# Performance work log

Hardware: AMD Instinct MI355X
Metric: run time of the kernel (lower is better)

## Reference

```python
import jax, jax.numpy as jnp
import numpy as np

ALPHA = 2.0
BETA = 50.0
BASE = 0.5
MARGIN = 0.1

B, D = 8192, 128
NUM_CLASSES = 512


def setup_inputs() -> dict:
    key = jax.random.key(0)
    k1, k2 = jax.random.split(key)
    emb = jax.random.normal(k1, (B, D), dtype=jnp.float32)
    emb = emb / jnp.linalg.norm(emb, axis=1, keepdims=True)  # unit-norm embeddings (standard for MS loss)
    labels = jax.random.randint(k2, (B,), 0, NUM_CLASSES, dtype=jnp.int64)
    return {"emb": emb, "labels": labels}


def reference(emb, labels):
    # sim: [B, B] similarity matrix
    sim = emb @ emb.T
    n = emb.shape[0]
    eq = labels[:, None] == labels[None, :]
    eye = jnp.eye(n, dtype=bool)
    pos = eq & ~eye          # positive pairs, diagonal removed
    neg = ~eq                # negative pairs

    # per-row hard-mining thresholds
    pos_min = jnp.min(jnp.where(pos, sim, jnp.inf), axis=1)    # min positive sim per row
    neg_max = jnp.max(jnp.where(neg, sim, -jnp.inf), axis=1)   # max negative sim per row

    neg_hard = neg & (sim + MARGIN > pos_min[:, None])
    pos_hard = pos & (sim - MARGIN < neg_max[:, None])

    # fallback: if mining selects nothing in a row, use all pos/neg (matches torch code)
    neg_sel = jnp.where(jnp.any(neg_hard, axis=1, keepdims=True), neg_hard, neg)
    pos_sel = jnp.where(jnp.any(pos_hard, axis=1, keepdims=True), pos_hard, pos)

    pos_loss = jnp.log1p(jnp.sum(jnp.where(pos_sel, jnp.exp(-ALPHA * (sim - BASE)), 0.0), axis=1)) / ALPHA
    neg_loss = jnp.log1p(jnp.sum(jnp.where(neg_sel, jnp.exp(BETA * (sim - BASE)), 0.0), axis=1)) / BETA

    valid = jnp.any(pos, axis=1) & jnp.any(neg, axis=1)  # rows skipped in torch loop
    row_loss = pos_loss + neg_loss
    num_valid = jnp.maximum(jnp.sum(valid.astype(jnp.float32)), 1.0)
    return jnp.sum(jnp.where(valid, row_loss, 0.0)) / num_valid
```

## Files before the change

kernel.cpp:

```cpp
#include <hip/hip_runtime.h>
#include <hip/hip_bf16.h>

#define NROW 8192
#define NDIM 128
#define CTILE 64
#define CCHUNK 8
#define RBLK 128
#define CAP 64
#define NCLS 512

typedef __attribute__((ext_vector_type(8))) short short8;
typedef __attribute__((ext_vector_type(4))) float f32x4;
typedef __attribute__((address_space(1))) const unsigned int guint;
typedef __attribute__((address_space(3))) unsigned int luint;

__device__ __forceinline__ unsigned f2u_mono(float f) {
  unsigned u = __float_as_uint(f);
  return (u & 0x80000000u) ? ~u : (u | 0x80000000u);
}
__device__ __forceinline__ float u2f_mono(unsigned u) {
  return __uint_as_float((u & 0x80000000u) ? (u ^ 0x80000000u) : ~u);
}
__device__ __forceinline__ unsigned short f2bf(float f) {
  unsigned u = __float_as_uint(f);
  u += 0x7fffu + ((u >> 16) & 1u);
  return (unsigned short)(u >> 16);
}

__global__ __launch_bounds__(256) void k_pre(
    const float* __restrict__ emb, const int* __restrict__ labels,
    unsigned short* __restrict__ h,
    unsigned* __restrict__ nmaxu, float* __restrict__ anb, float* __restrict__ hnb,
    float* __restrict__ pmin, float* __restrict__ apb, int* __restrict__ rcnt,
    float* __restrict__ pcache, unsigned* __restrict__ done_partial) {
  __shared__ float Le[CAP][NDIM + 1];
  __shared__ int rows_s[CAP];
  __shared__ int scnt;

  const int t = threadIdx.x;
  const int c = blockIdx.x;
  const int gid = c * 256 + t;

  if (gid < NROW) {
    nmaxu[gid] = 0u;
    anb[gid] = 0.f;
    hnb[gid] = 0.f;
  }
  if (c == 0 && t < 3) done_partial[t] = 0u;

  {
    int i = gid * 8;
    float4 f0 = *reinterpret_cast<const float4*>(emb + i);
    float4 f1 = *reinterpret_cast<const float4*>(emb + i + 4);
    ushort4 a, b;
    a.x = f2bf(f0.x); a.y = f2bf(f0.y); a.z = f2bf(f0.z); a.w = f2bf(f0.w);
    b.x = f2bf(f1.x); b.y = f2bf(f1.y); b.z = f2bf(f1.z); b.w = f2bf(f1.w);
    *reinterpret_cast<ushort4*>(h + i) = a;
    *reinterpret_cast<ushort4*>(h + i + 4) = b;
  }

  if (t == 0) scnt = 0;
  __syncthreads();
#pragma unroll
  for (int it = 0; it < NROW / 256; ++it) {
    const int row = it * 256 + t;
    if (labels[row] == c) {
      const int idx = atomicAdd(&scnt, 1);
      if (idx < CAP) rows_s[idx] = row;
    }
  }
  __syncthreads();
  const int cnt = min(scnt, CAP);
  if (cnt == 0) return;

  for (int idx = t; idx < cnt * NDIM; idx += 256) {
    const int k = idx >> 7, d = idx & 127;
    Le[k][d] = emb[(size_t)rows_s[k] * NDIM + d];
  }
  __syncthreads();

  const int il = t >> 4, jl = t & 15;
  for (int ib = 0; ib < cnt; ib += 16) {
    const int i = ib + il;
    float pm = INFINITY, apv = 0.f;
    for (int jb = 0; jb < cnt; jb += 16) {
      const int j = jb + jl;
      float p = INFINITY;
      if (i < cnt && j < cnt) {
        if (i != j) {
          float s = 0.f;
#pragma unroll 8
          for (int d = 0; d < NDIM; ++d) s = fmaf(Le[i][d], Le[j][d], s);
          p = s;
        }
        pcache[(size_t)rows_s[i] * CAP + j] = p;
        if (i != j) {
          pm = fminf(pm, p);
          apv += exp2f(fmaf(p, -2.885390082f, 1.442695041f));
        }
      }
    }
    pm = fminf(pm, __shfl_xor(pm, 1)); pm = fminf(pm, __shfl_xor(pm, 2));
    pm = fminf(pm, __shfl_xor(pm, 4)); pm = fminf(pm, __shfl_xor(pm, 8));
    apv += __shfl_xor(apv, 1); apv += __shfl_xor(apv, 2);
    apv += __shfl_xor(apv, 4); apv += __shfl_xor(apv, 8);
    if (jl == 0 && i < cnt) {
      pmin[rows_s[i]] = pm;
      apb[rows_s[i]] = apv;
      rcnt[rows_s[i]] = cnt;
    }
  }
}

__device__ __forceinline__ void stage_tile(const unsigned short* __restrict__ eh,
                                           int colBase, int t,
                                           unsigned short* __restrict__ Lbuf) {
#pragma unroll
  for (int it = 0; it < 4; ++it) {
    const int idx = it * 256 + t;
    const int r = idx >> 4;
    const int c = idx & 15;
    const int q = c ^ (r & 15);
    const unsigned short* src = eh + (size_t)(colBase + r) * NDIM + q * 8;
    unsigned short* dst = Lbuf + r * NDIM + c * 8;
    __builtin_amdgcn_global_load_lds((guint*)src, (luint*)dst, 16, 0, 0);
  }
}

__device__ __forceinline__ void mfma_from_lds(const unsigned short* __restrict__ Lbuf,
                                              const short8 (&bv)[4][2],
                                              const f32x4& Z,
                                              int g, int l15,
                                              f32x4 (&acc)[4][2]) {
#pragma unroll
  for (int kk = 0; kk < 4; ++kk) {
    short8 av[4];
#pragma unroll
    for (int m = 0; m < 4; ++m) {
      const int R = m * 16 + l15;
      const int pc = (kk * 4 + g) ^ l15;
      av[m] = *reinterpret_cast<const short8*>(Lbuf + R * NDIM + pc * 8);
    }
#pragma unroll
    for (int m = 0; m < 4; ++m)
#pragma unroll
      for (int n = 0; n < 2; ++n)
        acc[m][n] = __builtin_amdgcn_mfma_f32_16x16x32_bf16(
            av[m], bv[kk][n], (kk == 0) ? Z : acc[m][n], 0, 0, 0);
  }
}

__global__ __launch_bounds__(256, 3) void k_neg(
    const unsigned short* __restrict__ eh, const int* __restrict__ labels,
    const float* __restrict__ pmin, unsigned* __restrict__ nmaxu,
    float* __restrict__ anb, float* __restrict__ hnb) {
  __shared__ unsigned short L[2][CTILE * NDIM];

  const int t = threadIdx.x;
  const int lane = t & 63;
  const int wid = t >> 6;
  const int g = lane >> 4;
  const int l15 = lane & 15;
  const int rowBase = blockIdx.y * RBLK;
  const int col0 = blockIdx.x * CCHUNK * CTILE;

  stage_tile(eh, col0, t, L[0]);

  short8 bv[4][2];
  int lr[2];
  float thrn[2];
#pragma unroll
  for (int n = 0; n < 2; ++n) {
    const int grow = rowBase + wid * 32 + n * 16 + l15;
    lr[n] = labels[grow];
    thrn[n] = pmin[grow] - 0.1f;
#pragma unroll
    for (int kk = 0; kk < 4; ++kk)
      bv[kk][n] = *reinterpret_cast<const short8*>(eh + (size_t)grow * NDIM + kk * 32 + g * 8);
  }

  float nmaxA[2] = {-INFINITY, -INFINITY};
  float anA[2] = {0.f, 0.f}, hnA[2] = {0.f, 0.f};
  const f32x4 Z = {0.f, 0.f, 0.f, 0.f};

  asm volatile("s_waitcnt vmcnt(0)");
  __syncthreads();

  f32x4 acc[4][2];
  int cur = 0;
  for (int tt = 0; tt < CCHUNK; ++tt) {
    const int colBase = col0 + tt * CTILE;
    if (tt + 1 < CCHUNK) stage_tile(eh, colBase + CTILE, t, L[cur ^ 1]);
    int4 lcv[4];
#pragma unroll
    for (int m = 0; m < 4; ++m)
      lcv[m] = *reinterpret_cast<const int4*>(labels + colBase + m * 16 + g * 4);
    mfma_from_lds(L[cur], bv, Z, g, l15, acc);
#pragma unroll
    for (int n = 0; n < 2; ++n) {
#pragma unroll
      for (int m = 0; m < 4; ++m) {
#pragma unroll
        for (int r = 0; r < 4; ++r) {
          const float s = acc[m][n][r];
          const int lc = (r == 0) ? lcv[m].x : (r == 1) ? lcv[m].y
                        : (r == 2) ? lcv[m].z : lcv[m].w;
          const float x = (lr[n] == lc) ? -INFINITY : s;
          nmaxA[n] = fmaxf(nmaxA[n], x);
          const float e = exp2f(fmaf(x, 72.13475205f, -36.06737602f));
          anA[n] += e;
          hnA[n] += (x > thrn[n]) ? e : 0.f;
        }
      }
    }
    asm volatile("s_waitcnt vmcnt(0)");
    __syncthreads();
    cur ^= 1;
  }

#pragma unroll
  for (int n = 0; n < 2; ++n) {
    const int grow = rowBase + wid * 32 + n * 16 + l15;
    float nm = nmaxA[n], a0 = anA[n], a1 = hnA[n];
    nm = fmaxf(nm, __shfl_xor(nm, 16)); nm = fmaxf(nm, __shfl_xor(nm, 32));
    a0 += __shfl_xor(a0, 16); a0 += __shfl_xor(a0, 32);
    a1 += __shfl_xor(a1, 16); a1 += __shfl_xor(a1, 32);
    if (g == 0 && nm > -INFINITY) atomicMax(&nmaxu[grow], f2u_mono(nm));
    if (g == 1 && a0 > 0.f) atomicAdd(&anb[grow], a0);
    if (g == 2 && a1 > 0.f) atomicAdd(&hnb[grow], a1);
  }
}

__global__ __launch_bounds__(256) void k_final(
    const int* __restrict__ rcnt, const unsigned* __restrict__ nmaxu,
    const float* __restrict__ pcache, const float* __restrict__ apb,
    const float* __restrict__ anb, const float* __restrict__ hnb,
    unsigned* __restrict__ done_partial, float* __restrict__ out) {
  unsigned* done = done_partial;
  float* partial = (float*)(done_partial + 1);
  const int t = threadIdx.x;
  const int row = blockIdx.x * 256 + t;
  const int cnt = min(rcnt[row], CAP);
  const float thrp = u2f_mono(nmaxu[row]) + 0.1f;
  float hp = 0.f;
  for (int j = 0; j < cnt; ++j) {
    const float p = pcache[(size_t)row * CAP + j];
    hp += (p < thrp) ? exp2f(fmaf(p, -2.885390082f, 1.442695041f)) : 0.f;
  }
  const float ap = apb[row], an = anb[row], hn = hnb[row];
  const bool valid = (ap > 0.f) && (an > 0.f);
  const float ps = (hp > 0.f) ? hp : ap;
  const float ns = (hn > 0.f) ? hn : an;
  float acc = valid ? (0.5f * log1pf(ps) + 0.02f * log1pf(ns)) : 0.f;
  float cntv = valid ? 1.f : 0.f;
#pragma unroll
  for (int o = 32; o > 0; o >>= 1) {
    acc += __shfl_down(acc, o);
    cntv += __shfl_down(cntv, o);
  }
  __shared__ float sa[4], sc[4];
  const int w = t >> 6, lane = t & 63;
  if (lane == 0) { sa[w] = acc; sc[w] = cntv; }
  __syncthreads();
  if (t == 0) {
    atomicAdd(&partial[0], sa[0] + sa[1] + sa[2] + sa[3]);
    atomicAdd(&partial[1], sc[0] + sc[1] + sc[2] + sc[3]);
    __threadfence();
    if (atomicAdd(done, 1u) == (unsigned)(NROW / 256 - 1)) {
      const float A = atomicAdd(&partial[0], 0.f);
      const float C = atomicAdd(&partial[1], 0.f);
      out[0] = A / fmaxf(C, 1.f);
    }
  }
}

extern "C" void kernel_launch(void* const* d_in, const int* in_sizes, int n_in,
                              void* d_out, int out_size, void* d_ws, size_t ws_size,
                              hipStream_t stream) {
  const float* emb = (const float*)d_in[0];
  const int* labels = (const int*)d_in[1];
  float* out = (float*)d_out;

  unsigned short* embh = (unsigned short*)d_ws;
  float* pmin = (float*)((char*)d_ws + (size_t)NROW * NDIM * 2);
  float* apb = pmin + NROW;
  unsigned* nmaxu = (unsigned*)(apb + NROW);
  float* anb = (float*)(nmaxu + NROW);
  float* hnb = anb + NROW;
  int* rcnt = (int*)(hnb + NROW);
  unsigned* done_partial = (unsigned*)(rcnt + NROW);
  float* pcache = (float*)(done_partial + 4);

  k_pre<<<NCLS, 256, 0, stream>>>(emb, labels, embh, nmaxu, anb, hnb,
                                  pmin, apb, rcnt, pcache, done_partial);
  dim3 grid(NROW / (CTILE * CCHUNK), NROW / RBLK);
  k_neg<<<grid, 256, 0, stream>>>(embh, labels, pmin, nmaxu, anb, hnb);
  k_final<<<NROW / 256, 256, 0, stream>>>(rcnt, nmaxu, pcache,
                                          apb, anb, hnb, done_partial, out);
}
```

Measured before the change: 66.68 us.

## Restructure k_neg into single-wave blocks with barrier-free vmcnt-gated double buffering

```diff
diff --git a/kernel.cpp b/kernel.cpp
--- a/kernel.cpp
+++ b/kernel.cpp
@@ -3,9 +3,9 @@
 
 #define NROW 8192
 #define NDIM 128
-#define CTILE 64
-#define CCHUNK 8
-#define RBLK 128
+#define CTILE 32
+#define NTILE 16
+#define RWAVE 64
 #define CAP 64
 #define NCLS 512
 
@@ -116,8 +116,8 @@
                                            int colBase, int t,
                                            unsigned short* __restrict__ Lbuf) {
 #pragma unroll
-  for (int it = 0; it < 4; ++it) {
-    const int idx = it * 256 + t;
+  for (int it = 0; it < 8; ++it) {
+    const int idx = it * 64 + t;
     const int r = idx >> 4;
     const int c = idx & 15;
     const int q = c ^ (r & 15);
@@ -127,79 +127,79 @@
   }
 }
 
-__device__ __forceinline__ void mfma_from_lds(const unsigned short* __restrict__ Lbuf,
-                                              const short8 (&bv)[4][2],
-                                              const f32x4& Z,
-                                              int g, int l15,
-                                              f32x4 (&acc)[4][2]) {
-#pragma unroll
-  for (int kk = 0; kk < 4; ++kk) {
-    short8 av[4];
-#pragma unroll
-    for (int m = 0; m < 4; ++m) {
-      const int R = m * 16 + l15;
-      const int pc = (kk * 4 + g) ^ l15;
-      av[m] = *reinterpret_cast<const short8*>(Lbuf + R * NDIM + pc * 8);
-    }
-#pragma unroll
-    for (int m = 0; m < 4; ++m)
-#pragma unroll
-      for (int n = 0; n < 2; ++n)
-        acc[m][n] = __builtin_amdgcn_mfma_f32_16x16x32_bf16(
-            av[m], bv[kk][n], (kk == 0) ? Z : acc[m][n], 0, 0, 0);
-  }
-}
-
-__global__ __launch_bounds__(256, 3) void k_neg(
+__global__ __launch_bounds__(64) void k_neg(
     const unsigned short* __restrict__ eh, const int* __restrict__ labels,
     const float* __restrict__ pmin, unsigned* __restrict__ nmaxu,
     float* __restrict__ anb, float* __restrict__ hnb) {
   __shared__ unsigned short L[2][CTILE * NDIM];
 
   const int t = threadIdx.x;
-  const int lane = t & 63;
-  const int wid = t >> 6;
-  const int g = lane >> 4;
-  const int l15 = lane & 15;
-  const int rowBase = blockIdx.y * RBLK;
-  const int col0 = blockIdx.x * CCHUNK * CTILE;
-
-  stage_tile(eh, col0, t, L[0]);
-
-  short8 bv[4][2];
-  int lr[2];
-  float thrn[2];
-#pragma unroll
-  for (int n = 0; n < 2; ++n) {
-    const int grow = rowBase + wid * 32 + n * 16 + l15;
+  const int g = t >> 4;
+  const int l15 = t & 15;
+  const int rowBase = blockIdx.y * RWAVE;
+  const int col0 = blockIdx.x * NTILE * CTILE;
+
+  short8 bv[4][4];
+  int lr[4];
+  float thrn[4];
+#pragma unroll
+  for (int n = 0; n < 4; ++n) {
+    const int grow = rowBase + n * 16 + l15;
     lr[n] = labels[grow];
     thrn[n] = pmin[grow] - 0.1f;
 #pragma unroll
     for (int kk = 0; kk < 4; ++kk)
       bv[kk][n] = *reinterpret_cast<const short8*>(eh + (size_t)grow * NDIM + kk * 32 + g * 8);
   }
-
-  float nmaxA[2] = {-INFINITY, -INFINITY};
-  float anA[2] = {0.f, 0.f}, hnA[2] = {0.f, 0.f};
+  asm volatile("s_waitcnt vmcnt(0)" ::: "memory");
+
+  stage_tile(eh, col0, t, L[0]);
+
+  float nmaxA[4] = {-INFINITY, -INFINITY, -INFINITY, -INFINITY};
+  float anA[4] = {0.f, 0.f, 0.f, 0.f}, hnA[4] = {0.f, 0.f, 0.f, 0.f};
   const f32x4 Z = {0.f, 0.f, 0.f, 0.f};
 
-  asm volatile("s_waitcnt vmcnt(0)");
-  __syncthreads();
-
-  f32x4 acc[4][2];
   int cur = 0;
-  for (int tt = 0; tt < CCHUNK; ++tt) {
+  for (int tt = 0; tt < NTILE; ++tt) {
     const int colBase = col0 + tt * CTILE;
-    if (tt + 1 < CCHUNK) stage_tile(eh, colBase + CTILE, t, L[cur ^ 1]);
-    int4 lcv[4];
-#pragma unroll
-    for (int m = 0; m < 4; ++m)
+    const bool more = (tt + 1 < NTILE);
+    if (more) stage_tile(eh, colBase + CTILE, t, L[cur ^ 1]);
+    int4 lcv[2];
+#pragma unroll
+    for (int m = 0; m < 2; ++m)
       lcv[m] = *reinterpret_cast<const int4*>(labels + colBase + m * 16 + g * 4);
-    mfma_from_lds(L[cur], bv, Z, g, l15, acc);
-#pragma unroll
-    for (int n = 0; n < 2; ++n) {
-#pragma unroll
-      for (int m = 0; m < 4; ++m) {
+    if (more) asm volatile("s_waitcnt vmcnt(10)" ::: "memory");
+    else      asm volatile("s_waitcnt vmcnt(2)" ::: "memory");
+    __builtin_amdgcn_sched_barrier(0);
+
+    f32x4 acc[2][4];
+    __builtin_amdgcn_s_setprio(1);
+#pragma unroll
+    for (int kk = 0; kk < 4; ++kk) {
+      short8 av[2];
+#pragma unroll
+      for (int m = 0; m < 2; ++m) {
+        const int R = m * 16 + l15;
+        const int pc = (kk * 4 + g) ^ l15;
+        av[m] = *reinterpret_cast<const short8*>(L[cur] + R * NDIM + pc * 8);
+      }
+#pragma unroll
+      for (int m = 0; m < 2; ++m)
+#pragma unroll
+        for (int n = 0; n < 4; ++n)
+          acc[m][n] = __builtin_amdgcn_mfma_f32_16x16x32_bf16(
+              av[m], bv[kk][n], (kk == 0) ? Z : acc[m][n], 0, 0, 0);
+    }
+    __builtin_amdgcn_s_setprio(0);
+
+    if (more) asm volatile("s_waitcnt vmcnt(8)" ::: "memory");
+    else      asm volatile("s_waitcnt vmcnt(0)" ::: "memory");
+    __builtin_amdgcn_sched_barrier(0);
+
+#pragma unroll
+    for (int n = 0; n < 4; ++n) {
+#pragma unroll
+      for (int m = 0; m < 2; ++m) {
 #pragma unroll
         for (int r = 0; r < 4; ++r) {
           const float s = acc[m][n][r];
@@ -213,14 +213,12 @@
         }
       }
     }
-    asm volatile("s_waitcnt vmcnt(0)");
-    __syncthreads();
     cur ^= 1;
   }
 
 #pragma unroll
-  for (int n = 0; n < 2; ++n) {
-    const int grow = rowBase + wid * 32 + n * 16 + l15;
+  for (int n = 0; n < 4; ++n) {
+    const int grow = rowBase + n * 16 + l15;
     float nm = nmaxA[n], a0 = anA[n], a1 = hnA[n];
     nm = fmaxf(nm, __shfl_xor(nm, 16)); nm = fmaxf(nm, __shfl_xor(nm, 32));
     a0 += __shfl_xor(a0, 16); a0 += __shfl_xor(a0, 32);
@@ -293,8 +291,8 @@
 
   k_pre<<<NCLS, 256, 0, stream>>>(emb, labels, embh, nmaxu, anb, hnb,
                                   pmin, apb, rcnt, pcache, done_partial);
-  dim3 grid(NROW / (CTILE * CCHUNK), NROW / RBLK);
-  k_neg<<<grid, 256, 0, stream>>>(embh, labels, pmin, nmaxu, anb, hnb);
+  dim3 grid(NROW / (CTILE * NTILE), NROW / RWAVE);
+  k_neg<<<grid, 64, 0, stream>>>(embh, labels, pmin, nmaxu, anb, hnb);
   k_final<<<NROW / 256, 256, 0, stream>>>(rcnt, nmaxu, pcache,
                                           apb, anb, hnb, done_partial, out);
 }
```

Measured after the change: 81.16 us. 1.22x slower.
